# Kernel tuning notes

Hardware: AMD Instinct MI355X
Metric: run time of the kernel (lower is better)

## Reference

```python
import jax, jax.numpy as jnp
import numpy as np

B, T, E, H, Dh = 1, 2048, 1024, 16, 64
ROPE_BASE = 10000.0
NUM_BLOCK = 12  # transformer depth, only used for fc_2 init scale


def setup_inputs() -> dict:
    key = jax.random.key(0)
    k1, k2, k3 = jax.random.split(key, 3)
    x = jax.random.normal(k1, (B, T, E), dtype=jnp.float32)
    W1 = jax.random.normal(k2, (3 * E, E), dtype=jnp.float32) * 0.02
    W2 = jax.random.normal(k3, (E, E), dtype=jnp.float32) * (0.02 / np.sqrt(2.0 * NUM_BLOCK))
    return {"x": x, "W1": W1, "W2": W2}


def _rope(t):
    # t: (B, T, H, Dh). Rotate-half RoPE with base 10000.
    half = Dh // 2
    inv_freq = 1.0 / (ROPE_BASE ** (jnp.arange(0, half, dtype=jnp.float32) / half))
    ang = jnp.arange(T, dtype=jnp.float32)[:, None] * inv_freq[None, :]  # (T, half)
    cos = jnp.cos(ang)[None, :, None, :]
    sin = jnp.sin(ang)[None, :, None, :]
    t1, t2 = t[..., :half], t[..., half:]
    return jnp.concatenate([t1 * cos - t2 * sin, t2 * cos + t1 * sin], axis=-1)


def reference(x, W1, W2):
    # fused QKV projection
    qkv = x @ W1.T                                   # (B, T, 3E)
    q, k, v = jnp.split(qkv, 3, axis=-1)
    q = q.reshape(B, T, H, Dh)
    k = k.reshape(B, T, H, Dh)
    v = v.reshape(B, T, H, Dh)
    q = _rope(q)
    k = _rope(k)
    # causal attention (block-sparse flex-attention == per-sample causal mask)
    scale = 1.0 / np.sqrt(Dh)
    scores = jnp.einsum('bthd,bshd->bhts', q, k) * scale   # (B, H, T, T)
    causal = jnp.tril(jnp.ones((T, T), dtype=bool))
    scores = jnp.where(causal[None, None], scores, jnp.finfo(scores.dtype).min)
    p = jax.nn.softmax(scores, axis=-1)
    o = jnp.einsum('bhts,bshd->bthd', p, v).reshape(B, T, E)
    return o @ W2.T
```

## Files before the change

kernel.cpp:

```cpp
#include <hip/hip_runtime.h>
#include <math.h>

#define TT 2048
#define EE 1024
#define HH 16
#define DH 64

typedef unsigned short u16;
typedef __attribute__((ext_vector_type(8))) short bf16x8;
typedef __attribute__((ext_vector_type(4))) float f32x4;
typedef __attribute__((address_space(1))) unsigned int uint_g;
typedef __attribute__((address_space(3))) unsigned int uint_l;

__device__ __forceinline__ u16 f2bf(float f) {
  unsigned u = __float_as_uint(f);
  u += 0x7fffu + ((u >> 16) & 1u);
  return (u16)(u >> 16);
}

__global__ __launch_bounds__(256) void cvt_bf16(const float* __restrict__ s,
                                                u16* __restrict__ d, int n8) {
  int i = blockIdx.x * 256 + threadIdx.x;
  if (i >= n8) return;
  const float4* s4 = (const float4*)s;
  float4 a = s4[2 * i], b = s4[2 * i + 1];
  bf16x8 o;
  o[0] = (short)f2bf(a.x); o[1] = (short)f2bf(a.y);
  o[2] = (short)f2bf(a.z); o[3] = (short)f2bf(a.w);
  o[4] = (short)f2bf(b.x); o[5] = (short)f2bf(b.y);
  o[6] = (short)f2bf(b.z); o[7] = (short)f2bf(b.w);
  *(bf16x8*)&d[8 * i] = o;
}

template <int EPI>
__global__ __launch_bounds__(256) void gemm_mfma(
    const u16* __restrict__ A, const u16* __restrict__ B, float* __restrict__ C,
    float* __restrict__ qb, float* __restrict__ kb, u16* __restrict__ vt,
    int M, int N, int K) {
  __shared__ u16 smem[8192];
  const int tid = threadIdx.x;
  const int lane = tid & 63;
  const int wid = tid >> 6;
  const int wr = wid >> 1, wc = wid & 1;
  const int m0 = blockIdx.y * 128, n0 = blockIdx.x * 128;

  const u16* gp[4];
  int lo[4];
#pragma unroll
  for (int q = 0; q < 4; q++) {
    int o = (wid * 4 + q) * 1024 + lane * 16;
    lo[q] = o >> 1;
    if (o < 8192) {
      int row = o >> 6, col = (o >> 1) & 31;
      gp[q] = A + (size_t)(m0 + row) * K + col;
    } else {
      int o2 = o - 8192;
      int row = o2 >> 6, col = (o2 >> 1) & 31;
      gp[q] = B + (size_t)(n0 + row) * K + col;
    }
  }

  const int a_off = (wr * 64 + (lane & 15)) * 32 + (lane >> 4) * 8;
  const int b_off = 4096 + (wc * 64 + (lane & 15)) * 32 + (lane >> 4) * 8;

  f32x4 acc[4][4];
#pragma unroll
  for (int i = 0; i < 4; i++)
#pragma unroll
    for (int j = 0; j < 4; j++) acc[i][j] = f32x4{0.f, 0.f, 0.f, 0.f};

  for (int k0 = 0; k0 < K; k0 += 32) {
    __syncthreads();
#pragma unroll
    for (int q = 0; q < 4; q++) {
      __builtin_amdgcn_global_load_lds((const uint_g*)gp[q],
                                       (uint_l*)&smem[lo[q]], 16, 0, 0);
      gp[q] += 32;
    }
    __syncthreads();
    bf16x8 af[4], bg[4];
#pragma unroll
    for (int i = 0; i < 4; i++) af[i] = *(const bf16x8*)&smem[a_off + i * 512];
#pragma unroll
    for (int j = 0; j < 4; j++) bg[j] = *(const bf16x8*)&smem[b_off + j * 512];
#pragma unroll
    for (int i = 0; i < 4; i++)
#pragma unroll
      for (int j = 0; j < 4; j++)
        acc[i][j] = __builtin_amdgcn_mfma_f32_16x16x32_bf16(af[i], bg[j],
                                                            acc[i][j], 0, 0, 0);
  }

  const int rbase = (lane >> 4) * 4;
  const int ncol = lane & 15;
  if (EPI == 0) {
#pragma unroll
    for (int i = 0; i < 4; i++) {
      int m = m0 + wr * 64 + i * 16 + rbase;
#pragma unroll
      for (int j = 0; j < 4; j++) {
        int n = n0 + wc * 64 + j * 16 + ncol;
#pragma unroll
        for (int r = 0; r < 4; r++) C[(size_t)(m + r) * N + n] = acc[i][j][r];
      }
    }
  } else {
#pragma unroll
    for (int j = 0; j < 4; j++) {
      int n = n0 + wc * 64 + j * 16 + ncol;
      int which = n >> 10, h = (n >> 6) & 15, d = n & 63;
#pragma unroll
      for (int i = 0; i < 4; i++) {
        int m = m0 + wr * 64 + i * 16 + rbase;
        if (which == 2) {
#pragma unroll
          for (int r = 0; r < 4; r++)
            vt[((size_t)h * DH + d) * TT + m + r] = f2bf(acc[i][j][r]);
        } else {
          float* dst = (which == 0) ? qb : kb;
#pragma unroll
          for (int r = 0; r < 4; r++)
            dst[((size_t)h * TT + m + r) * DH + d] = acc[i][j][r];
        }
      }
    }
  }
}

__global__ void rope_table(float* __restrict__ cs, float* __restrict__ sn) {
  int i = blockIdx.x * 256 + threadIdx.x;
  int t = i >> 5;
  int d = i & 31;
  float inv = powf(10000.f, -((float)d) / 32.f);
  float ang = (float)t * inv;
  cs[i] = (float)cos((double)ang);
  sn[i] = (float)sin((double)ang);
}

__global__ void rope_apply_bf16(const float* __restrict__ qb,
                                const float* __restrict__ kb,
                                u16* __restrict__ q16, u16* __restrict__ k16,
                                const float* __restrict__ cs,
                                const float* __restrict__ sn) {
  int id = blockIdx.x * 256 + threadIdx.x;
  const int n = HH * TT * 32;
  int which = id >= n;
  int i = which ? id - n : id;
  const float* p = which ? kb : qb;
  u16* dst = which ? k16 : q16;
  int h = i >> 16;
  int rem = i & 65535;
  size_t off = ((size_t)h * TT) * DH + (size_t)(rem >> 5) * DH + (rem & 31);
  float c = cs[rem];
  float s = sn[rem];
  float a = p[off];
  float b = p[off + 32];
  dst[off] = f2bf(a * c - b * s);
  dst[off + 32] = f2bf(b * c + a * s);
}

__global__ __launch_bounds__(256) void attn_mfma(
    const u16* __restrict__ Q, const u16* __restrict__ K,
    const u16* __restrict__ Vt, u16* __restrict__ O) {
  __shared__ u16 P_lds[64][72];
  const int tid = threadIdx.x;
  const int lane = tid & 63;
  const int wid = tid >> 6;
  const int l15 = lane & 15;
  const int l4 = lane >> 4;
  const int rbase = l4 * 4;
  const int h = blockIdx.x & 15;
  const int idx = blockIdx.x >> 4;
  const int tile = (idx < 16) ? idx : 47 - idx;
  const int qbase = tile << 6;
  const int nc = tile + 1;

  const u16* Qh = Q + (size_t)h * TT * DH;
  const u16* Kh = K + (size_t)h * TT * DH;
  const u16* Vh = Vt + (size_t)h * DH * TT;

  const int qrow = qbase + wid * 16 + l15;
  bf16x8 qf0 = *(const bf16x8*)&Qh[(size_t)qrow * DH + l4 * 8];
  bf16x8 qf1 = *(const bf16x8*)&Qh[(size_t)qrow * DH + 32 + l4 * 8];

  float m[4], l[4];
  f32x4 oacc[4];
#pragma unroll
  for (int r = 0; r < 4; r++) {
    m[r] = -1e30f;
    l[r] = 0.f;
  }
#pragma unroll
  for (int j = 0; j < 4; j++) oacc[j] = f32x4{0.f, 0.f, 0.f, 0.f};

  for (int ch = 0; ch < nc; ch++) {
    const int kbase = ch << 6;
    f32x4 s[4];
#pragma unroll
    for (int j = 0; j < 4; j++) s[j] = f32x4{0.f, 0.f, 0.f, 0.f};
#pragma unroll
    for (int j = 0; j < 4; j++) {
      bf16x8 kf0 =
          *(const bf16x8*)&Kh[(size_t)(kbase + j * 16 + l15) * DH + l4 * 8];
      bf16x8 kf1 = *(const bf16x8*)&Kh[(size_t)(kbase + j * 16 + l15) * DH +
                                       32 + l4 * 8];
      s[j] = __builtin_amdgcn_mfma_f32_16x16x32_bf16(qf0, kf0, s[j], 0, 0, 0);
      s[j] = __builtin_amdgcn_mfma_f32_16x16x32_bf16(qf1, kf1, s[j], 0, 0, 0);
    }
#pragma unroll
    for (int j = 0; j < 4; j++) {
      s[j][0] *= 0.125f; s[j][1] *= 0.125f;
      s[j][2] *= 0.125f; s[j][3] *= 0.125f;
    }
    if (ch == tile) {
#pragma unroll
      for (int j = 0; j < 4; j++) {
        int kg = kbase + j * 16 + l15;
#pragma unroll
        for (int r = 0; r < 4; r++) {
          int qg = qbase + wid * 16 + rbase + r;
          if (kg > qg) s[j][r] = -1e30f;
        }
      }
    }
#pragma unroll
    for (int r = 0; r < 4; r++) {
      float rm = fmaxf(fmaxf(s[0][r], s[1][r]), fmaxf(s[2][r], s[3][r]));
      rm = fmaxf(rm, __shfl_xor(rm, 1));
      rm = fmaxf(rm, __shfl_xor(rm, 2));
      rm = fmaxf(rm, __shfl_xor(rm, 4));
      rm = fmaxf(rm, __shfl_xor(rm, 8));
      const float mn = fmaxf(m[r], rm);
      const float corr = __expf(m[r] - mn);
      m[r] = mn;
      float rs = 0.f;
#pragma unroll
      for (int j = 0; j < 4; j++) {
        float p = __expf(s[j][r] - mn);
        s[j][r] = p;
        rs += p;
      }
      rs += __shfl_xor(rs, 1);
      rs += __shfl_xor(rs, 2);
      rs += __shfl_xor(rs, 4);
      rs += __shfl_xor(rs, 8);
      l[r] = l[r] * corr + rs;
      oacc[0][r] *= corr;
      oacc[1][r] *= corr;
      oacc[2][r] *= corr;
      oacc[3][r] *= corr;
    }
    const int prow0 = wid * 16 + rbase;
#pragma unroll
    for (int j = 0; j < 4; j++)
#pragma unroll
      for (int r = 0; r < 4; r++)
        P_lds[prow0 + r][j * 16 + l15] = f2bf(s[j][r]);
#pragma unroll
    for (int ks = 0; ks < 2; ks++) {
      bf16x8 pa = *(const bf16x8*)&P_lds[wid * 16 + l15][ks * 32 + l4 * 8];
#pragma unroll
      for (int j = 0; j < 4; j++) {
        bf16x8 vf = *(const bf16x8*)&Vh[(size_t)(j * 16 + l15) * TT + kbase +
                                        ks * 32 + l4 * 8];
        oacc[j] =
            __builtin_amdgcn_mfma_f32_16x16x32_bf16(pa, vf, oacc[j], 0, 0, 0);
      }
    }
  }
#pragma unroll
  for (int r = 0; r < 4; r++) {
    const float inv = 1.f / l[r];
    const int qg = qbase + wid * 16 + rbase + r;
#pragma unroll
    for (int j = 0; j < 4; j++)
      O[(size_t)qg * EE + h * DH + j * 16 + l15] = f2bf(oacc[j][r] * inv);
  }
}

extern "C" void kernel_launch(void* const* d_in, const int* in_sizes, int n_in,
                              void* d_out, int out_size, void* d_ws,
                              size_t ws_size, hipStream_t stream) {
  const float* x = (const float*)d_in[0];
  const float* W1 = (const float*)d_in[1];
  const float* W2 = (const float*)d_in[2];
  float* out = (float*)d_out;

  float* ws = (float*)d_ws;
  const size_t HTD = (size_t)HH * TT * DH;
  float* qb = ws;
  float* kb = qb + HTD;
  float* cs = kb + HTD;
  float* sn = cs + (size_t)TT * 32;
  u16* qb16 = (u16*)(sn + (size_t)TT * 32);
  u16* kb16 = qb16 + HTD;
  u16* vt16 = kb16 + HTD;
  u16* obb = vt16 + HTD;
  u16* xb = obb + (size_t)TT * EE;
  u16* w1b = xb + (size_t)TT * EE;
  u16* w2b = w1b + (size_t)3 * EE * EE;

  const int n8x = TT * EE / 8, n8w1 = 3 * EE * EE / 8, n8w2 = EE * EE / 8;
  cvt_bf16<<<(n8x + 255) / 256, 256, 0, stream>>>(x, xb, n8x);
  cvt_bf16<<<(n8w1 + 255) / 256, 256, 0, stream>>>(W1, w1b, n8w1);
  cvt_bf16<<<(n8w2 + 255) / 256, 256, 0, stream>>>(W2, w2b, n8w2);
  rope_table<<<(TT * 32) / 256, 256, 0, stream>>>(cs, sn);
  gemm_mfma<1><<<dim3(3 * EE / 128, TT / 128), 256, 0, stream>>>(
      xb, w1b, nullptr, qb, kb, vt16, TT, 3 * EE, EE);
  rope_apply_bf16<<<(2 * HH * TT * 32) / 256, 256, 0, stream>>>(
      qb, kb, qb16, kb16, cs, sn);
  attn_mfma<<<512, 256, 0, stream>>>(qb16, kb16, vt16, obb);
  gemm_mfma<0><<<dim3(EE / 128, TT / 128), 256, 0, stream>>>(
      obb, w2b, out, nullptr, nullptr, nullptr, TT, EE, EE);
}
```

Before: 205.6 us.

## Fuse RoPE into QKV GEMM epilogue, merge conversions, shrink attention blocks

Applies RoPE directly in the QKV GEMM epilogue, pairing accumulator tiles j and j+2 (d and d+32 within a head), so Q/K go straight to bf16. This removes the fp32 Q/K round trip and the separate rope_apply kernel. The three fp32-to-bf16 conversion launches become one kernel. Attention moves from 64-row, 4-wave blocks to 16-row single-wave blocks ordered heaviest-first, trading less K/V reuse per block for finer load balancing and more blocks in flight.

```diff
diff --git a/kernel.cpp b/kernel.cpp
--- a/kernel.cpp
+++ b/kernel.cpp
@@ -18,10 +18,20 @@
   return (u16)(u >> 16);
 }
 
-__global__ __launch_bounds__(256) void cvt_bf16(const float* __restrict__ s,
-                                                u16* __restrict__ d, int n8) {
+__global__ __launch_bounds__(256) void cvt_all(
+    const float* __restrict__ x, const float* __restrict__ W1,
+    const float* __restrict__ W2, u16* __restrict__ xb, u16* __restrict__ w1b,
+    u16* __restrict__ w2b) {
   int i = blockIdx.x * 256 + threadIdx.x;
-  if (i >= n8) return;
+  const float* s;
+  u16* d;
+  if (i < 262144) {
+    s = x; d = xb;
+  } else if (i < 262144 + 393216) {
+    i -= 262144; s = W1; d = w1b;
+  } else {
+    i -= 262144 + 393216; s = W2; d = w2b;
+  }
   const float4* s4 = (const float4*)s;
   float4 a = s4[2 * i], b = s4[2 * i + 1];
   bf16x8 o;
@@ -32,11 +42,22 @@
   *(bf16x8*)&d[8 * i] = o;
 }
 
+__global__ void rope_table(float* __restrict__ cs, float* __restrict__ sn) {
+  int i = blockIdx.x * 256 + threadIdx.x;
+  int t = i >> 5;
+  int d = i & 31;
+  float inv = powf(10000.f, -((float)d) / 32.f);
+  float ang = (float)t * inv;
+  cs[i] = (float)cos((double)ang);
+  sn[i] = (float)sin((double)ang);
+}
+
 template <int EPI>
 __global__ __launch_bounds__(256) void gemm_mfma(
     const u16* __restrict__ A, const u16* __restrict__ B, float* __restrict__ C,
-    float* __restrict__ qb, float* __restrict__ kb, u16* __restrict__ vt,
-    int M, int N, int K) {
+    u16* __restrict__ q16, u16* __restrict__ k16, u16* __restrict__ vt,
+    const float* __restrict__ cs, const float* __restrict__ sn, int M, int N,
+    int K) {
   __shared__ u16 smem[8192];
   const int tid = threadIdx.x;
   const int lane = tid & 63;
@@ -105,81 +126,64 @@
       }
     }
   } else {
-#pragma unroll
-    for (int j = 0; j < 4; j++) {
-      int n = n0 + wc * 64 + j * 16 + ncol;
-      int which = n >> 10, h = (n >> 6) & 15, d = n & 63;
-#pragma unroll
-      for (int i = 0; i < 4; i++) {
-        int m = m0 + wr * 64 + i * 16 + rbase;
-        if (which == 2) {
+    const int which = n0 >> 10;
+    if (which == 2) {
+#pragma unroll
+      for (int j = 0; j < 4; j++) {
+        int n = n0 + wc * 64 + j * 16 + ncol;
+        int h = (n >> 6) & 15, d = n & 63;
+#pragma unroll
+        for (int i = 0; i < 4; i++) {
+          int m = m0 + wr * 64 + i * 16 + rbase;
 #pragma unroll
           for (int r = 0; r < 4; r++)
             vt[((size_t)h * DH + d) * TT + m + r] = f2bf(acc[i][j][r]);
-        } else {
-          float* dst = (which == 0) ? qb : kb;
-#pragma unroll
-          for (int r = 0; r < 4; r++)
-            dst[((size_t)h * TT + m + r) * DH + d] = acc[i][j][r];
         }
       }
-    }
-  }
-}
-
-__global__ void rope_table(float* __restrict__ cs, float* __restrict__ sn) {
-  int i = blockIdx.x * 256 + threadIdx.x;
-  int t = i >> 5;
-  int d = i & 31;
-  float inv = powf(10000.f, -((float)d) / 32.f);
-  float ang = (float)t * inv;
-  cs[i] = (float)cos((double)ang);
-  sn[i] = (float)sin((double)ang);
-}
-
-__global__ void rope_apply_bf16(const float* __restrict__ qb,
-                                const float* __restrict__ kb,
-                                u16* __restrict__ q16, u16* __restrict__ k16,
-                                const float* __restrict__ cs,
-                                const float* __restrict__ sn) {
-  int id = blockIdx.x * 256 + threadIdx.x;
-  const int n = HH * TT * 32;
-  int which = id >= n;
-  int i = which ? id - n : id;
-  const float* p = which ? kb : qb;
-  u16* dst = which ? k16 : q16;
-  int h = i >> 16;
-  int rem = i & 65535;
-  size_t off = ((size_t)h * TT) * DH + (size_t)(rem >> 5) * DH + (rem & 31);
-  float c = cs[rem];
-  float s = sn[rem];
-  float a = p[off];
-  float b = p[off + 32];
-  dst[off] = f2bf(a * c - b * s);
-  dst[off + 32] = f2bf(b * c + a * s);
-}
-
-__global__ __launch_bounds__(256) void attn_mfma(
+    } else {
+      u16* dst = (which == 0) ? q16 : k16;
+#pragma unroll
+      for (int j = 0; j < 2; j++) {
+        int n = n0 + wc * 64 + j * 16 + ncol;
+        int h = (n >> 6) & 15, d = n & 63;
+#pragma unroll
+        for (int i = 0; i < 4; i++) {
+          int mrow = m0 + wr * 64 + i * 16 + rbase;
+#pragma unroll
+          for (int r = 0; r < 4; r++) {
+            int t = mrow + r;
+            float c = cs[t * 32 + d];
+            float s = sn[t * 32 + d];
+            float a = acc[i][j][r];
+            float b = acc[i][j + 2][r];
+            size_t off = ((size_t)h * TT + t) * DH + d;
+            dst[off] = f2bf(a * c - b * s);
+            dst[off + 32] = f2bf(b * c + a * s);
+          }
+        }
+      }
+    }
+  }
+}
+
+__global__ __launch_bounds__(64) void attn_mfma(
     const u16* __restrict__ Q, const u16* __restrict__ K,
     const u16* __restrict__ Vt, u16* __restrict__ O) {
-  __shared__ u16 P_lds[64][72];
-  const int tid = threadIdx.x;
-  const int lane = tid & 63;
-  const int wid = tid >> 6;
+  __shared__ u16 P_lds[16][72];
+  const int lane = threadIdx.x;
   const int l15 = lane & 15;
   const int l4 = lane >> 4;
   const int rbase = l4 * 4;
   const int h = blockIdx.x & 15;
-  const int idx = blockIdx.x >> 4;
-  const int tile = (idx < 16) ? idx : 47 - idx;
-  const int qbase = tile << 6;
-  const int nc = tile + 1;
+  const int tile = 127 - (blockIdx.x >> 4);
+  const int qbase = tile << 4;
+  const int nc = ((qbase + 15) >> 6) + 1;
 
   const u16* Qh = Q + (size_t)h * TT * DH;
   const u16* Kh = K + (size_t)h * TT * DH;
   const u16* Vh = Vt + (size_t)h * DH * TT;
 
-  const int qrow = qbase + wid * 16 + l15;
+  const int qrow = qbase + l15;
   bf16x8 qf0 = *(const bf16x8*)&Qh[(size_t)qrow * DH + l4 * 8];
   bf16x8 qf1 = *(const bf16x8*)&Qh[(size_t)qrow * DH + 32 + l4 * 8];
 
@@ -212,13 +216,13 @@
       s[j][0] *= 0.125f; s[j][1] *= 0.125f;
       s[j][2] *= 0.125f; s[j][3] *= 0.125f;
     }
-    if (ch == tile) {
+    if (ch == nc - 1) {
 #pragma unroll
       for (int j = 0; j < 4; j++) {
         int kg = kbase + j * 16 + l15;
 #pragma unroll
         for (int r = 0; r < 4; r++) {
-          int qg = qbase + wid * 16 + rbase + r;
+          int qg = qbase + rbase + r;
           if (kg > qg) s[j][r] = -1e30f;
         }
       }
@@ -250,15 +254,14 @@
       oacc[2][r] *= corr;
       oacc[3][r] *= corr;
     }
-    const int prow0 = wid * 16 + rbase;
 #pragma unroll
     for (int j = 0; j < 4; j++)
 #pragma unroll
       for (int r = 0; r < 4; r++)
-        P_lds[prow0 + r][j * 16 + l15] = f2bf(s[j][r]);
+        P_lds[rbase + r][j * 16 + l15] = f2bf(s[j][r]);
 #pragma unroll
     for (int ks = 0; ks < 2; ks++) {
-      bf16x8 pa = *(const bf16x8*)&P_lds[wid * 16 + l15][ks * 32 + l4 * 8];
+      bf16x8 pa = *(const bf16x8*)&P_lds[l15][ks * 32 + l4 * 8];
 #pragma unroll
       for (int j = 0; j < 4; j++) {
         bf16x8 vf = *(const bf16x8*)&Vh[(size_t)(j * 16 + l15) * TT + kbase +
@@ -271,7 +274,7 @@
 #pragma unroll
   for (int r = 0; r < 4; r++) {
     const float inv = 1.f / l[r];
-    const int qg = qbase + wid * 16 + rbase + r;
+    const int qg = qbase + rbase + r;
 #pragma unroll
     for (int j = 0; j < 4; j++)
       O[(size_t)qg * EE + h * DH + j * 16 + l15] = f2bf(oacc[j][r] * inv);
@@ -288,9 +291,7 @@
 
   float* ws = (float*)d_ws;
   const size_t HTD = (size_t)HH * TT * DH;
-  float* qb = ws;
-  float* kb = qb + HTD;
-  float* cs = kb + HTD;
+  float* cs = ws;
   float* sn = cs + (size_t)TT * 32;
   u16* qb16 = (u16*)(sn + (size_t)TT * 32);
   u16* kb16 = qb16 + HTD;
@@ -300,16 +301,11 @@
   u16* w1b = xb + (size_t)TT * EE;
   u16* w2b = w1b + (size_t)3 * EE * EE;
 
-  const int n8x = TT * EE / 8, n8w1 = 3 * EE * EE / 8, n8w2 = EE * EE / 8;
-  cvt_bf16<<<(n8x + 255) / 256, 256, 0, stream>>>(x, xb, n8x);
-  cvt_bf16<<<(n8w1 + 255) / 256, 256, 0, stream>>>(W1, w1b, n8w1);
-  cvt_bf16<<<(n8w2 + 255) / 256, 256, 0, stream>>>(W2, w2b, n8w2);
   rope_table<<<(TT * 32) / 256, 256, 0, stream>>>(cs, sn);
+  cvt_all<<<786432 / 256, 256, 0, stream>>>(x, W1, W2, xb, w1b, w2b);
   gemm_mfma<1><<<dim3(3 * EE / 128, TT / 128), 256, 0, stream>>>(
-      xb, w1b, nullptr, qb, kb, vt16, TT, 3 * EE, EE);
-  rope_apply_bf16<<<(2 * HH * TT * 32) / 256, 256, 0, stream>>>(
-      qb, kb, qb16, kb16, cs, sn);
-  attn_mfma<<<512, 256, 0, stream>>>(qb16, kb16, vt16, obb);
+      xb, w1b, nullptr, qb16, kb16, vt16, cs, sn, TT, 3 * EE, EE);
+  attn_mfma<<<2048, 64, 0, stream>>>(qb16, kb16, vt16, obb);
   gemm_mfma<0><<<dim3(EE / 128, TT / 128), 256, 0, stream>>>(
-      obb, w2b, out, nullptr, nullptr, nullptr, TT, EE, EE);
-}
+      obb, w2b, out, nullptr, nullptr, nullptr, nullptr, nullptr, TT, EE, EE);
+}
```

New measurement: 201.9 us. About the same (-1.8%).
